# Performance work log

Measured on AMD Instinct MI355X. Metric: run time of the kernel, lower is better.

## Reference

```python
import jax, jax.numpy as jnp
import numpy as np

# Model/config constants (from init_kwargs / input shapes)
NUM_HEADS = 32
HEAD_DIM = 128
NUM_KV = 8
SCALE = 0.08838834764831845  # 1/sqrt(128)
NUM_BLOCKS = 4096
BLOCK_SIZE = 16
BLOCKS_PER_SEQ = 64
BATCH = 64
GROUP = NUM_HEADS // NUM_KV  # num_queries_per_kv


def setup_inputs() -> dict:
    key = jax.random.key(0)
    ks = jax.random.split(key, 6)
    q = jax.random.normal(ks[0], (BATCH, NUM_HEADS, HEAD_DIM), dtype=jnp.float32)
    k = jax.random.normal(ks[1], (BATCH, NUM_KV, HEAD_DIM), dtype=jnp.float32)
    v = jax.random.normal(ks[2], (BATCH, NUM_KV, HEAD_DIM), dtype=jnp.float32)
    k_cache = jax.random.normal(ks[3], (NUM_BLOCKS, BLOCK_SIZE, NUM_KV, HEAD_DIM), dtype=jnp.float32)
    v_cache = jax.random.normal(ks[4], (NUM_BLOCKS, BLOCK_SIZE, NUM_KV, HEAD_DIM), dtype=jnp.float32)
    # one new token per sequence; unique slots -> deterministic scatter
    slot_mapping = jnp.arange(BATCH, dtype=jnp.int32)
    block_tables = jax.random.randint(ks[5], (BATCH, BLOCKS_PER_SEQ), 0, NUM_BLOCKS, dtype=jnp.int32)
    return {"q": q, "k": k, "v": v, "k_cache": k_cache, "v_cache": v_cache,
            "slot_mapping": slot_mapping, "block_tables": block_tables}


def reference(q, k, v, k_cache, v_cache, slot_mapping, block_tables):
    kv_flat = NUM_KV * HEAD_DIM
    # --- cache update: scatter new K/V rows into flattened paged cache ---
    kc = k_cache.reshape(-1, kv_flat).at[slot_mapping].set(k.reshape(-1, kv_flat))
    vc = v_cache.reshape(-1, kv_flat).at[slot_mapping].set(v.reshape(-1, kv_flat))
    kc = kc.reshape(NUM_BLOCKS, BLOCK_SIZE, NUM_KV, HEAD_DIM)
    vc = vc.reshape(NUM_BLOCKS, BLOCK_SIZE, NUM_KV, HEAD_DIM)
    # --- block-table gather: [B, blocks_per_seq, block_size, KV, D] -> [B, S, KV, D] ---
    K = kc[block_tables].reshape(BATCH, BLOCKS_PER_SEQ * BLOCK_SIZE, NUM_KV, HEAD_DIM)
    V = vc[block_tables].reshape(BATCH, BLOCKS_PER_SEQ * BLOCK_SIZE, NUM_KV, HEAD_DIM)
    # --- GQA single-token attention (non-causal SDPA on one query) ---
    qg = q.reshape(BATCH, NUM_KV, GROUP, HEAD_DIM)  # group query heads per kv head
    scores = jnp.einsum('bkgd,bskd->bkgs', qg, K) * SCALE  # [B, KV, G, S]
    probs = jax.nn.softmax(scores, axis=-1)
    o = jnp.einsum('bkgs,bskd->bkgd', probs, V)  # [B, KV, G, D]
    return o.reshape(BATCH, NUM_HEADS * HEAD_DIM)
```

## Files before the change

### kernel.cpp

```cpp
#include <hip/hip_runtime.h>

constexpr int NUM_HEADS      = 32;
constexpr int HEAD_DIM       = 128;
constexpr int NUM_KV         = 8;
constexpr int GROUP          = 4;
constexpr int BLOCK_SIZE     = 16;
constexpr int BLOCKS_PER_SEQ = 64;
constexpr int BATCH          = 64;
constexpr int SEQ            = BLOCKS_PER_SEQ * BLOCK_SIZE;
constexpr int KV_ROW         = NUM_KV * HEAD_DIM;
constexpr int SPLIT          = 8;
constexpr int TOK            = SEQ / SPLIT;
constexpr int BLKS           = TOK / BLOCK_SIZE;
constexpr float SCALE        = 0.08838834764831845f;

constexpr size_t WS_O = 0;
constexpr size_t WS_M = (size_t)BATCH * NUM_KV * SPLIT * GROUP * HEAD_DIM;
constexpr size_t WS_L = WS_M + (size_t)BATCH * NUM_KV * SPLIT * GROUP;

__global__ __launch_bounds__(256) void paged_attn_split(
    const float* __restrict__ q,
    const float* __restrict__ knew,
    const float* __restrict__ vnew,
    const float* __restrict__ kcache,
    const float* __restrict__ vcache,
    const int*   __restrict__ slot_mapping,
    const int*   __restrict__ block_tables,
    float*       __restrict__ ws)
{
    const int wg  = (int)blockIdx.x;
    const int sp  = wg & (SPLIT - 1);
    const int bk  = wg >> 3;
    const int kvh = bk & 7;
    const int b   = bk >> 3;
    const int tid = (int)threadIdx.x;
    const int lane = tid & 63;
    const int wave = tid >> 6;

    __shared__ int   s_row[TOK];
    __shared__ float s_p[TOK][GROUP];
    __shared__ float s_o[4][GROUP][HEAD_DIM];
    __shared__ int   s_bt[BLKS];
    __shared__ int   s_slot[BATCH];

    if (tid < BLKS) s_bt[tid] = block_tables[b * BLOCKS_PER_SEQ + sp * BLKS + tid];
    if (tid >= 64 && tid < 64 + BATCH) s_slot[tid - 64] = slot_mapping[tid - 64];
    __syncthreads();

    if (tid < TOK) {
        int slot = s_bt[tid >> 4] * BLOCK_SIZE + (tid & 15);
        int r = slot;
        #pragma unroll
        for (int i = 0; i < BATCH; ++i)
            if (s_slot[i] == slot) r = -1 - i;
        s_row[tid] = r;
    }

    const int h0 = kvh * GROUP;
    const size_t hoff = (size_t)kvh * HEAD_DIM;
    const int sub = lane >> 4;
    const int sl  = lane & 15;

    float4 qa[GROUP], qb[GROUP];
    #pragma unroll
    for (int g = 0; g < GROUP; ++g) {
        const float* qp = q + ((size_t)b * NUM_HEADS + h0 + g) * HEAD_DIM + sl * 8;
        qa[g] = *reinterpret_cast<const float4*>(qp);
        qb[g] = *reinterpret_cast<const float4*>(qp + 4);
    }
    __syncthreads();

    #pragma unroll
    for (int t = wave * 4 + sub; t < TOK; t += 16) {
        int r = s_row[t];
        const float* krow = (r >= 0)
            ? kcache + (size_t)r * KV_ROW + hoff
            : knew   + (size_t)(-1 - r) * KV_ROW + hoff;
        float4 ka = *reinterpret_cast<const float4*>(krow + sl * 8);
        float4 kb = *reinterpret_cast<const float4*>(krow + sl * 8 + 4);
        float p[GROUP];
        #pragma unroll
        for (int g = 0; g < GROUP; ++g) {
            p[g] = qa[g].x * ka.x + qa[g].y * ka.y + qa[g].z * ka.z + qa[g].w * ka.w
                 + qb[g].x * kb.x + qb[g].y * kb.y + qb[g].z * kb.z + qb[g].w * kb.w;
        }
        #pragma unroll
        for (int off = 1; off < 16; off <<= 1) {
            #pragma unroll
            for (int g = 0; g < GROUP; ++g) p[g] += __shfl_xor(p[g], off);
        }
        if (sl == 0) {
            #pragma unroll
            for (int g = 0; g < GROUP; ++g) s_p[t][g] = p[g] * SCALE;
        }
    }
    __syncthreads();

    {
        const int g = wave;
        float v0 = s_p[lane][g], v1 = s_p[lane + 64][g];
        float m = fmaxf(v0, v1);
        #pragma unroll
        for (int off = 32; off; off >>= 1) m = fmaxf(m, __shfl_xor(m, off));
        float e0 = __expf(v0 - m), e1 = __expf(v1 - m);
        s_p[lane][g] = e0;
        s_p[lane + 64][g] = e1;
        float sum = e0 + e1;
        #pragma unroll
        for (int off = 32; off; off >>= 1) sum += __shfl_xor(sum, off);
        if (lane == 0) {
            ws[WS_M + (size_t)wg * GROUP + g] = m;
            ws[WS_L + (size_t)wg * GROUP + g] = sum;
        }
    }
    __syncthreads();

    {
        const int half = lane >> 5;
        const int dl   = lane & 31;
        float4 a0 = {0,0,0,0}, a1 = a0, a2 = a0, a3 = a0;
        #pragma unroll 8
        for (int i = 0; i < TOK / 8; ++i) {
            int t = wave * (TOK / 4) + i * 2 + half;
            int r = s_row[t];
            const float* vrow = (r >= 0)
                ? vcache + (size_t)r * KV_ROW + hoff
                : vnew   + (size_t)(-1 - r) * KV_ROW + hoff;
            float4 vv = *reinterpret_cast<const float4*>(vrow + dl * 4);
            float4 pv = *reinterpret_cast<const float4*>(&s_p[t][0]);
            a0.x += pv.x * vv.x; a0.y += pv.x * vv.y; a0.z += pv.x * vv.z; a0.w += pv.x * vv.w;
            a1.x += pv.y * vv.x; a1.y += pv.y * vv.y; a1.z += pv.y * vv.z; a1.w += pv.y * vv.w;
            a2.x += pv.z * vv.x; a2.y += pv.z * vv.y; a2.z += pv.z * vv.z; a2.w += pv.z * vv.w;
            a3.x += pv.w * vv.x; a3.y += pv.w * vv.y; a3.z += pv.w * vv.z; a3.w += pv.w * vv.w;
        }
        #define RED4(A) A.x += __shfl_xor(A.x, 32); A.y += __shfl_xor(A.y, 32); \
                        A.z += __shfl_xor(A.z, 32); A.w += __shfl_xor(A.w, 32);
        RED4(a0) RED4(a1) RED4(a2) RED4(a3)
        #undef RED4
        if (half == 0) {
            *reinterpret_cast<float4*>(&s_o[wave][0][dl * 4]) = a0;
            *reinterpret_cast<float4*>(&s_o[wave][1][dl * 4]) = a1;
            *reinterpret_cast<float4*>(&s_o[wave][2][dl * 4]) = a2;
            *reinterpret_cast<float4*>(&s_o[wave][3][dl * 4]) = a3;
        }
    }
    __syncthreads();

    {
        const int g = wave;
        const int d = lane * 2;
        float ox = 0.f, oy = 0.f;
        #pragma unroll
        for (int w = 0; w < 4; ++w) {
            ox += s_o[w][g][d];
            oy += s_o[w][g][d + 1];
        }
        *reinterpret_cast<float2*>(
            ws + WS_O + ((size_t)wg * GROUP + g) * HEAD_DIM + d) = make_float2(ox, oy);
    }
}

__global__ __launch_bounds__(128) void paged_attn_combine(
    const float* __restrict__ ws, float* __restrict__ out)
{
    const int hb  = (int)blockIdx.x;
    const int g   = hb & 3;
    const int bk  = hb >> 2;
    const int kvh = bk & 7;
    const int b   = bk >> 3;
    const int d   = (int)threadIdx.x;

    float m[SPLIT];
    float mstar = -1e30f;
    #pragma unroll
    for (int s = 0; s < SPLIT; ++s) {
        m[s] = ws[WS_M + ((size_t)(bk * SPLIT + s) * GROUP) + g];
        mstar = fmaxf(mstar, m[s]);
    }
    float L = 0.f, acc = 0.f;
    #pragma unroll
    for (int s = 0; s < SPLIT; ++s) {
        float w = __expf(m[s] - mstar);
        L   += w * ws[WS_L + ((size_t)(bk * SPLIT + s) * GROUP) + g];
        acc += w * ws[WS_O + ((size_t)(bk * SPLIT + s) * GROUP + g) * HEAD_DIM + d];
    }
    out[((size_t)b * NUM_HEADS + kvh * GROUP + g) * HEAD_DIM + d] = acc / L;
}

extern "C" void kernel_launch(void* const* d_in, const int* in_sizes, int n_in,
                              void* d_out, int out_size, void* d_ws, size_t ws_size,
                              hipStream_t stream) {
    const float* q    = (const float*)d_in[0];
    const float* knew = (const float*)d_in[1];
    const float* vnew = (const float*)d_in[2];
    const float* kc   = (const float*)d_in[3];
    const float* vc   = (const float*)d_in[4];
    const int*   slot = (const int*)d_in[5];
    const int*   bt   = (const int*)d_in[6];
    float* out = (float*)d_out;
    float* ws  = (float*)d_ws;

    hipLaunchKernelGGL(paged_attn_split, dim3(BATCH * NUM_KV * SPLIT), dim3(256),
                       0, stream, q, knew, vnew, kc, vc, slot, bt, ws);
    hipLaunchKernelGGL(paged_attn_combine, dim3(BATCH * NUM_KV * GROUP), dim3(128),
                       0, stream, ws, out);
}
```

Measured before the change: 85.92 us.

## Make split-kernel phases wave-local and merge per-wave softmax with LSE rescaling

Each wave now handles its own contiguous slice of tokens for row lookup, QK scores, softmax and PV accumulation, removing the intermediate block-wide barriers. Per-wave max and sum are kept in shared memory and merged with exponential rescaling before the partial output is written. The slot lookup now reads slot_mapping directly from global with vector loads instead of staging it in shared memory. This aims to let waves progress independently and overlap memory latency, at the cost of some extra rescale arithmetic and redundant global reads of small tables.

```diff
diff --git a/kernel.cpp b/kernel.cpp
--- a/kernel.cpp
+++ b/kernel.cpp
@@ -11,7 +11,7 @@
 constexpr int KV_ROW         = NUM_KV * HEAD_DIM;
 constexpr int SPLIT          = 8;
 constexpr int TOK            = SEQ / SPLIT;
-constexpr int BLKS           = TOK / BLOCK_SIZE;
+constexpr int TPW            = TOK / 4;
 constexpr float SCALE        = 0.08838834764831845f;
 
 constexpr size_t WS_O = 0;
@@ -35,25 +35,27 @@
     const int b   = bk >> 3;
     const int tid = (int)threadIdx.x;
     const int lane = tid & 63;
-    const int wave = tid >> 6;
-
-    __shared__ int   s_row[TOK];
-    __shared__ float s_p[TOK][GROUP];
+    const int w    = tid >> 6;
+
+    __shared__ int   s_row[4][TPW];
+    __shared__ float s_p[4][TPW][GROUP];
     __shared__ float s_o[4][GROUP][HEAD_DIM];
-    __shared__ int   s_bt[BLKS];
-    __shared__ int   s_slot[BATCH];
-
-    if (tid < BLKS) s_bt[tid] = block_tables[b * BLOCKS_PER_SEQ + sp * BLKS + tid];
-    if (tid >= 64 && tid < 64 + BATCH) s_slot[tid - 64] = slot_mapping[tid - 64];
-    __syncthreads();
-
-    if (tid < TOK) {
-        int slot = s_bt[tid >> 4] * BLOCK_SIZE + (tid & 15);
+    __shared__ float s_ml[4][GROUP][2];
+
+    if (lane < TPW) {
+        int t   = w * TPW + lane;
+        int blk = block_tables[b * BLOCKS_PER_SEQ + sp * (TOK / BLOCK_SIZE) + (t >> 4)];
+        int slot = blk * BLOCK_SIZE + (t & 15);
         int r = slot;
         #pragma unroll
-        for (int i = 0; i < BATCH; ++i)
-            if (s_slot[i] == slot) r = -1 - i;
-        s_row[tid] = r;
+        for (int i = 0; i < BATCH; i += 4) {
+            int4 sm = *reinterpret_cast<const int4*>(&slot_mapping[i]);
+            if (sm.x == slot) r = -1 - i;
+            if (sm.y == slot) r = -2 - i;
+            if (sm.z == slot) r = -3 - i;
+            if (sm.w == slot) r = -4 - i;
+        }
+        s_row[w][lane] = r;
     }
 
     const int h0 = kvh * GROUP;
@@ -68,11 +70,11 @@
         qa[g] = *reinterpret_cast<const float4*>(qp);
         qb[g] = *reinterpret_cast<const float4*>(qp + 4);
     }
-    __syncthreads();
-
-    #pragma unroll
-    for (int t = wave * 4 + sub; t < TOK; t += 16) {
-        int r = s_row[t];
+
+    #pragma unroll
+    for (int it = 0; it < TPW / 4; ++it) {
+        int t = it * 4 + sub;
+        int r = s_row[w][t];
         const float* krow = (r >= 0)
             ? kcache + (size_t)r * KV_ROW + hoff
             : knew   + (size_t)(-1 - r) * KV_ROW + hoff;
@@ -91,43 +93,41 @@
         }
         if (sl == 0) {
             #pragma unroll
-            for (int g = 0; g < GROUP; ++g) s_p[t][g] = p[g] * SCALE;
-        }
-    }
-    __syncthreads();
-
-    {
-        const int g = wave;
-        float v0 = s_p[lane][g], v1 = s_p[lane + 64][g];
-        float m = fmaxf(v0, v1);
-        #pragma unroll
-        for (int off = 32; off; off >>= 1) m = fmaxf(m, __shfl_xor(m, off));
-        float e0 = __expf(v0 - m), e1 = __expf(v1 - m);
-        s_p[lane][g] = e0;
-        s_p[lane + 64][g] = e1;
-        float sum = e0 + e1;
-        #pragma unroll
-        for (int off = 32; off; off >>= 1) sum += __shfl_xor(sum, off);
-        if (lane == 0) {
-            ws[WS_M + (size_t)wg * GROUP + g] = m;
-            ws[WS_L + (size_t)wg * GROUP + g] = sum;
-        }
-    }
-    __syncthreads();
+            for (int g = 0; g < GROUP; ++g) s_p[w][t][g] = p[g] * SCALE;
+        }
+    }
+
+    #pragma unroll
+    for (int gp = 0; gp < 2; ++gp) {
+        int g = gp * 2 + (lane >> 5);
+        float v = s_p[w][lane & 31][g];
+        float m = v;
+        #pragma unroll
+        for (int off = 1; off < 32; off <<= 1) m = fmaxf(m, __shfl_xor(m, off));
+        float e = __expf(v - m);
+        s_p[w][lane & 31][g] = e;
+        float s = e;
+        #pragma unroll
+        for (int off = 1; off < 32; off <<= 1) s += __shfl_xor(s, off);
+        if ((lane & 31) == 0) {
+            s_ml[w][g][0] = m;
+            s_ml[w][g][1] = s;
+        }
+    }
 
     {
         const int half = lane >> 5;
         const int dl   = lane & 31;
         float4 a0 = {0,0,0,0}, a1 = a0, a2 = a0, a3 = a0;
         #pragma unroll 8
-        for (int i = 0; i < TOK / 8; ++i) {
-            int t = wave * (TOK / 4) + i * 2 + half;
-            int r = s_row[t];
+        for (int i = 0; i < TPW / 2; ++i) {
+            int t = i * 2 + half;
+            int r = s_row[w][t];
             const float* vrow = (r >= 0)
                 ? vcache + (size_t)r * KV_ROW + hoff
                 : vnew   + (size_t)(-1 - r) * KV_ROW + hoff;
             float4 vv = *reinterpret_cast<const float4*>(vrow + dl * 4);
-            float4 pv = *reinterpret_cast<const float4*>(&s_p[t][0]);
+            float4 pv = *reinterpret_cast<const float4*>(&s_p[w][t][0]);
             a0.x += pv.x * vv.x; a0.y += pv.x * vv.y; a0.z += pv.x * vv.z; a0.w += pv.x * vv.w;
             a1.x += pv.y * vv.x; a1.y += pv.y * vv.y; a1.z += pv.y * vv.z; a1.w += pv.y * vv.w;
             a2.x += pv.z * vv.x; a2.y += pv.z * vv.y; a2.z += pv.z * vv.z; a2.w += pv.z * vv.w;
@@ -138,25 +138,43 @@
         RED4(a0) RED4(a1) RED4(a2) RED4(a3)
         #undef RED4
         if (half == 0) {
-            *reinterpret_cast<float4*>(&s_o[wave][0][dl * 4]) = a0;
-            *reinterpret_cast<float4*>(&s_o[wave][1][dl * 4]) = a1;
-            *reinterpret_cast<float4*>(&s_o[wave][2][dl * 4]) = a2;
-            *reinterpret_cast<float4*>(&s_o[wave][3][dl * 4]) = a3;
-        }
-    }
+            *reinterpret_cast<float4*>(&s_o[w][0][dl * 4]) = a0;
+            *reinterpret_cast<float4*>(&s_o[w][1][dl * 4]) = a1;
+            *reinterpret_cast<float4*>(&s_o[w][2][dl * 4]) = a2;
+            *reinterpret_cast<float4*>(&s_o[w][3][dl * 4]) = a3;
+        }
+    }
+
     __syncthreads();
 
     {
-        const int g = wave;
+        const int g = w;
+        float mw[4], lw[4], mc = -1e30f;
+        #pragma unroll
+        for (int u = 0; u < 4; ++u) {
+            mw[u] = s_ml[u][g][0];
+            lw[u] = s_ml[u][g][1];
+            mc = fmaxf(mc, mw[u]);
+        }
+        float ew[4], L = 0.f;
+        #pragma unroll
+        for (int u = 0; u < 4; ++u) {
+            ew[u] = __expf(mw[u] - mc);
+            L += ew[u] * lw[u];
+        }
         const int d = lane * 2;
         float ox = 0.f, oy = 0.f;
         #pragma unroll
-        for (int w = 0; w < 4; ++w) {
-            ox += s_o[w][g][d];
-            oy += s_o[w][g][d + 1];
+        for (int u = 0; u < 4; ++u) {
+            ox += ew[u] * s_o[u][g][d];
+            oy += ew[u] * s_o[u][g][d + 1];
         }
         *reinterpret_cast<float2*>(
             ws + WS_O + ((size_t)wg * GROUP + g) * HEAD_DIM + d) = make_float2(ox, oy);
+        if (lane == 0) {
+            ws[WS_M + (size_t)wg * GROUP + g] = mc;
+            ws[WS_L + (size_t)wg * GROUP + g] = L;
+        }
     }
 }
 
@@ -180,9 +198,9 @@
     float L = 0.f, acc = 0.f;
     #pragma unroll
     for (int s = 0; s < SPLIT; ++s) {
-        float w = __expf(m[s] - mstar);
-        L   += w * ws[WS_L + ((size_t)(bk * SPLIT + s) * GROUP) + g];
-        acc += w * ws[WS_O + ((size_t)(bk * SPLIT + s) * GROUP + g) * HEAD_DIM + d];
+        float wgt = __expf(m[s] - mstar);
+        L   += wgt * ws[WS_L + ((size_t)(bk * SPLIT + s) * GROUP) + g];
+        acc += wgt * ws[WS_O + ((size_t)(bk * SPLIT + s) * GROUP + g) * HEAD_DIM + d];
     }
     out[((size_t)b * NUM_HEADS + kvh * GROUP + g) * HEAD_DIM + d] = acc / L;
 }
```

After: 86.70 us. About the same (+0.9%).
